# Optimization experiments

Hardware: AMD Instinct MI355X
Metric: run time of the kernel (lower is better)

The kernel has to match this reference:

```python
import jax, jax.numpy as jnp
import numpy as np

N_NODES = 500000
N_EDGES = 8000000


def gcn_conv(x, W, b, src, dst, n_nodes):
    # PyG GCNConv: add self-loops, symmetric normalization, x@W, scatter-add.
    loop = jnp.arange(n_nodes, dtype=src.dtype)
    src_a = jnp.concatenate([src, loop])  # [E+N]
    dst_a = jnp.concatenate([dst, loop])
    deg = jax.ops.segment_sum(jnp.ones_like(dst_a, dtype=x.dtype), dst_a,
                              num_segments=n_nodes)  # in-degree incl. self-loop
    dinv = jnp.where(deg > 0, jax.lax.rsqrt(deg), 0.0)
    norm = dinv[src_a] * dinv[dst_a]  # [E+N]
    xw = x @ W  # [N, out]
    msg = xw[src_a] * norm[:, None]  # [E+N, out]
    out = jax.ops.segment_sum(msg, dst_a, num_segments=n_nodes)
    return out + b


def setup_inputs() -> dict:
    key = jax.random.key(0)
    k1, k2, k3, k4, k5, k6 = jax.random.split(key, 6)
    x = jax.random.uniform(k1, (N_NODES, 1), dtype=jnp.float32)
    edge_index = jax.random.randint(k2, (2, N_EDGES), 0, N_NODES, dtype=jnp.int32)
    W1 = jax.random.normal(k3, (1, 16), dtype=jnp.float32)
    b1 = jax.random.normal(k4, (16,), dtype=jnp.float32) * 0.1
    W2 = jax.random.normal(k5, (16, 2), dtype=jnp.float32)
    b2 = jax.random.normal(k6, (2,), dtype=jnp.float32) * 0.1
    return {"x": x, "edge_index": edge_index, "W1": W1, "b1": b1,
            "W2": W2, "b2": b2}


def reference(x, edge_index, W1, b1, W2, b2):
    src, dst = edge_index[0], edge_index[1]
    h = gcn_conv(x, W1, b1, src, dst, N_NODES)
    h = jax.nn.relu(h)
    # dropout is identity in eval mode
    h = gcn_conv(h, W2, b2, src, dst, N_NODES)
    return jax.nn.log_softmax(h, axis=1)
```

## Files before the change

kernel.cpp:

```cpp
#include <hip/hip_runtime.h>
#include <math.h>


typedef unsigned int uint4v __attribute__((ext_vector_type(4)));

#define NPB 1024
#define NPB_SHIFT 10
#define NPB_MASK (NPB - 1)
#define MAXB 512
#define P1T 512
#define CHUNK 16384
#define SORT_CAP 17408
#define SPT 17

__device__ __forceinline__ unsigned short f2bf(float f) {
    unsigned int x = __float_as_uint(f);
    x += 0x7fffu + ((x >> 16) & 1u);
    return (unsigned short)(x >> 16);
}
__device__ __forceinline__ float bf2f(unsigned short h) {
    return __uint_as_float((unsigned int)h << 16);
}

__global__ __launch_bounds__(P1T, 4) void k_bucket(
    const int* __restrict__ src, const int* __restrict__ dst,
    unsigned int* __restrict__ file, int* __restrict__ ctr,
    int E, int nbucket, int cap)
{
    __shared__ unsigned int sorted[CHUNK];
    __shared__ int cnt[MAXB];
    __shared__ int pre[MAXB + 1];
    __shared__ int gb[MAXB];
    __shared__ int rk[MAXB];

    const int t  = threadIdx.x;
    const int e0 = blockIdx.x * CHUNK;
    const int nE = min(CHUNK, E - e0);

    for (int b = t; b < MAXB; b += P1T) { cnt[b] = 0; rk[b] = 0; }
    __syncthreads();

    const bool full = (nE == CHUNK);
    int4 dc[8];

    if (full) {
        const int4* d4 = (const int4*)(dst + e0);
#pragma unroll
        for (int k = 0; k < 8; ++k) dc[k] = d4[t + k * P1T];
#pragma unroll
        for (int k = 0; k < 8; ++k) {
            atomicAdd(&cnt[((unsigned)dc[k].x) >> NPB_SHIFT], 1);
            atomicAdd(&cnt[((unsigned)dc[k].y) >> NPB_SHIFT], 1);
            atomicAdd(&cnt[((unsigned)dc[k].z) >> NPB_SHIFT], 1);
            atomicAdd(&cnt[((unsigned)dc[k].w) >> NPB_SHIFT], 1);
        }
    } else {
        for (int i = t; i < nE; i += P1T)
            atomicAdd(&cnt[((unsigned)dst[e0 + i]) >> NPB_SHIFT], 1);
    }
    __syncthreads();

    int v = (t < nbucket) ? cnt[t] : 0;
    pre[t + 1] = v;
    if (t == 0) pre[0] = 0;
    __syncthreads();
    for (int off = 1; off < P1T; off <<= 1) {
        int add = (t >= off) ? pre[t + 1 - off] : 0;
        __syncthreads();
        pre[t + 1] += add;
        __syncthreads();
    }

    for (int b = t; b < nbucket; b += P1T) {
        int c = cnt[b];
        gb[b] = c ? atomicAdd(&ctr[b], c) : 0;
    }
    __syncthreads();

    if (full) {
        const int4* s4 = (const int4*)(src + e0);
#pragma unroll
        for (int k = 0; k < 8; ++k) {
            int4 s = s4[t + k * P1T];
            int4 d = dc[k];
            {
                int b = ((unsigned)d.x) >> NPB_SHIFT;
                int r = atomicAdd(&rk[b], 1);
                sorted[pre[b] + r] = (((unsigned)s.x) << NPB_SHIFT) | ((unsigned)d.x & NPB_MASK);
            }
            {
                int b = ((unsigned)d.y) >> NPB_SHIFT;
                int r = atomicAdd(&rk[b], 1);
                sorted[pre[b] + r] = (((unsigned)s.y) << NPB_SHIFT) | ((unsigned)d.y & NPB_MASK);
            }
            {
                int b = ((unsigned)d.z) >> NPB_SHIFT;
                int r = atomicAdd(&rk[b], 1);
                sorted[pre[b] + r] = (((unsigned)s.z) << NPB_SHIFT) | ((unsigned)d.z & NPB_MASK);
            }
            {
                int b = ((unsigned)d.w) >> NPB_SHIFT;
                int r = atomicAdd(&rk[b], 1);
                sorted[pre[b] + r] = (((unsigned)s.w) << NPB_SHIFT) | ((unsigned)d.w & NPB_MASK);
            }
        }
    } else {
        for (int i = t; i < nE; i += P1T) {
            int d = dst[e0 + i];
            int b = ((unsigned)d) >> NPB_SHIFT;
            unsigned int w = (((unsigned)src[e0 + i]) << NPB_SHIFT) |
                             ((unsigned)d & NPB_MASK);
            int r = atomicAdd(&rk[b], 1);
            sorted[pre[b] + r] = w;
        }
    }
    __syncthreads();

    {
        const int wid  = t >> 6;
        const int lane = t & 63;
        const int nw   = P1T >> 6;
        for (int b = wid; b < nbucket; b += nw) {
            int s0 = pre[b], s1 = pre[b + 1];
            int base = gb[b];
            unsigned int* dp = file + (size_t)b * cap;
            for (int j = s0 + lane; j < s1; j += 64) {
                int idx = base + (j - s0);
                if (idx < cap)
                    __builtin_nontemporal_store(sorted[j], &dp[idx]);
            }
        }
    }
}

__global__ __launch_bounds__(NPB) void k_sort(
    unsigned int* __restrict__ file, const int* __restrict__ ctr,
    int* __restrict__ start, const float* __restrict__ x,
    float* __restrict__ dinv, unsigned short* __restrict__ u,
    int N, int cap)
{
    __shared__ unsigned int sorted[SORT_CAP];
    __shared__ int cnt[NPB];
    __shared__ int pre[NPB + 1];

    const int t = threadIdx.x;
    const int b = blockIdx.x;
    const int nb = min(ctr[b], cap);
    unsigned int* f = file + (size_t)b * cap;

    cnt[t] = 0;
    __syncthreads();

    unsigned int ev[SPT];
    int rk_[SPT];
#pragma unroll
    for (int k = 0; k < SPT; ++k) {
        int i = t + (k << NPB_SHIFT);
        if (i < nb) ev[k] = __builtin_nontemporal_load(f + i);
    }
#pragma unroll
    for (int k = 0; k < SPT; ++k) {
        int i = t + (k << NPB_SHIFT);
        if (i < nb) rk_[k] = atomicAdd(&cnt[ev[k] & NPB_MASK], 1);
    }
    __syncthreads();

    pre[t + 1] = cnt[t];
    if (t == 0) pre[0] = 0;
    __syncthreads();
    for (int off = 1; off < NPB; off <<= 1) {
        int add = (t >= off) ? pre[t + 1 - off] : 0;
        __syncthreads();
        pre[t + 1] += add;
        __syncthreads();
    }

#pragma unroll
    for (int k = 0; k < SPT; ++k) {
        int i = t + (k << NPB_SHIFT);
        if (i < nb)
            sorted[pre[ev[k] & NPB_MASK] + rk_[k]] = ev[k] >> NPB_SHIFT;
    }
    __syncthreads();

    for (int i = t; i < nb; i += NPB)
        __builtin_nontemporal_store(sorted[i], &f[i]);

    start[b * (NPB + 1) + t] = pre[t];
    if (t == 0) start[b * (NPB + 1) + NPB] = pre[NPB];

    const int g = b * NPB + t;
    if (g < N) {
        float dv = rsqrtf((float)(cnt[t] + 1));
        dinv[g] = dv;
        u[g] = f2bf(x[g] * dv);
    }
}

__global__ __launch_bounds__(256) void k_agg1(
    const unsigned int* __restrict__ file, const int* __restrict__ start,
    const unsigned short* __restrict__ u, const float* __restrict__ dinv,
    const float* __restrict__ W1, const float* __restrict__ b1,
    const float* __restrict__ W2, unsigned int* __restrict__ q,
    int N, int cap)
{
    int g = blockIdx.x * 256 + threadIdx.x;
    if (g >= N) return;
    int b = g >> NPB_SHIFT, loc = g & NPB_MASK;
    const int* st = start + b * (NPB + 1);
    int e0 = st[loc], e1 = st[loc + 1];
    const unsigned int* f = file + (size_t)b * cap;

    float acc = 0.f;
    int j = e0;
    for (; j + 4 <= e1; j += 4) {
        unsigned int s0 = f[j], s1 = f[j + 1], s2 = f[j + 2], s3 = f[j + 3];
        float a = bf2f(u[s0]), bb = bf2f(u[s1]);
        float c = bf2f(u[s2]), d = bf2f(u[s3]);
        acc += (a + bb) + (c + d);
    }
    for (; j < e1; ++j) acc += bf2f(u[f[j]]);

    float dv = dinv[g];
    float s1v = (acc + bf2f(u[g])) * dv;
    float c0 = 0.f, c1 = 0.f;
#pragma unroll
    for (int k = 0; k < 16; ++k) {
        float h = fmaxf(fmaf(s1v, W1[k], b1[k]), 0.f);
        c0 = fmaf(h, W2[2 * k], c0);
        c1 = fmaf(h, W2[2 * k + 1], c1);
    }
    q[g] = (unsigned int)f2bf(c0 * dv) | ((unsigned int)f2bf(c1 * dv) << 16);
}

__global__ __launch_bounds__(256) void k_agg2(
    const unsigned int* __restrict__ file, const int* __restrict__ start,
    const unsigned int* __restrict__ q, const float* __restrict__ dinv,
    const float* __restrict__ b2, float2* __restrict__ out,
    int N, int cap)
{
    int g = blockIdx.x * 256 + threadIdx.x;
    if (g >= N) return;
    int b = g >> NPB_SHIFT, loc = g & NPB_MASK;
    const int* st = start + b * (NPB + 1);
    int e0 = st[loc], e1 = st[loc + 1];
    const unsigned int* f = file + (size_t)b * cap;

    float a0 = 0.f, a1 = 0.f;
    int j = e0;
    for (; j + 4 <= e1; j += 4) {
        unsigned int g0 = q[f[j]], g1 = q[f[j + 1]];
        unsigned int g2 = q[f[j + 2]], g3 = q[f[j + 3]];
        a0 += (bf2f((unsigned short)g0) + bf2f((unsigned short)g1)) +
              (bf2f((unsigned short)g2) + bf2f((unsigned short)g3));
        a1 += (bf2f((unsigned short)(g0 >> 16)) + bf2f((unsigned short)(g1 >> 16))) +
              (bf2f((unsigned short)(g2 >> 16)) + bf2f((unsigned short)(g3 >> 16)));
    }
    for (; j < e1; ++j) {
        unsigned int gq = q[f[j]];
        a0 += bf2f((unsigned short)gq);
        a1 += bf2f((unsigned short)(gq >> 16));
    }

    float dv = dinv[g];
    unsigned int qi = q[g];
    float o0 = (a0 + bf2f((unsigned short)qi)) * dv + b2[0];
    float o1 = (a1 + bf2f((unsigned short)(qi >> 16))) * dv + b2[1];
    float m = fmaxf(o0, o1);
    float l = m + logf(expf(o0 - m) + expf(o1 - m));
    out[g] = make_float2(o0 - l, o1 - l);
}

#define NT 256
__global__ __launch_bounds__(NT) void fb_deg(const int* __restrict__ dst,
                                             int* __restrict__ deg, int E) {
    int e = blockIdx.x * blockDim.x + threadIdx.x;
    if (e < E) atomicAdd(&deg[dst[e]], 1);
}
__global__ __launch_bounds__(NT) void fb_node1(const float* __restrict__ x,
                                               const int* __restrict__ deg,
                                               float* __restrict__ dinv,
                                               float* __restrict__ u, int N) {
    int i = blockIdx.x * blockDim.x + threadIdx.x;
    if (i < N) {
        float dv = rsqrtf((float)(deg[i] + 1));
        dinv[i] = dv;
        u[i] = x[i] * dv;
    }
}
__global__ __launch_bounds__(NT) void fb_edge1(const int* __restrict__ src,
                                               const int* __restrict__ dst,
                                               const float* __restrict__ u,
                                               float* __restrict__ agg1, int E) {
    int e = blockIdx.x * blockDim.x + threadIdx.x;
    if (e < E) atomicAdd(&agg1[dst[e]], u[src[e]]);
}
__global__ __launch_bounds__(NT) void fb_node2(const float* __restrict__ agg1,
                                               const float* __restrict__ u,
                                               const float* __restrict__ dinv,
                                               const float* __restrict__ W1,
                                               const float* __restrict__ b1,
                                               const float* __restrict__ W2,
                                               float2* __restrict__ q, int N) {
    int i = blockIdx.x * blockDim.x + threadIdx.x;
    if (i < N) {
        float dv = dinv[i];
        float s1 = (agg1[i] + u[i]) * dv;
        float c0 = 0.f, c1 = 0.f;
#pragma unroll
        for (int k = 0; k < 16; ++k) {
            float h = fmaxf(fmaf(s1, W1[k], b1[k]), 0.f);
            c0 = fmaf(h, W2[2 * k], c0);
            c1 = fmaf(h, W2[2 * k + 1], c1);
        }
        q[i] = make_float2(c0 * dv, c1 * dv);
    }
}
__global__ __launch_bounds__(NT) void fb_edge2(const int* __restrict__ src,
                                               const int* __restrict__ dst,
                                               const float2* __restrict__ q,
                                               float* __restrict__ agg2, int E) {
    int e = blockIdx.x * blockDim.x + threadIdx.x;
    if (e < E) {
        float2 qq = q[src[e]];
        atomicAdd(&agg2[2 * dst[e]], qq.x);
        atomicAdd(&agg2[2 * dst[e] + 1], qq.y);
    }
}
__global__ __launch_bounds__(NT) void fb_node3(const float* __restrict__ agg2,
                                               const float2* __restrict__ q,
                                               const float* __restrict__ dinv,
                                               const float* __restrict__ b2,
                                               float2* __restrict__ out, int N) {
    int i = blockIdx.x * blockDim.x + threadIdx.x;
    if (i < N) {
        float dv = dinv[i];
        float2 qi = q[i];
        float o0 = (agg2[2 * i] + qi.x) * dv + b2[0];
        float o1 = (agg2[2 * i + 1] + qi.y) * dv + b2[1];
        float m = fmaxf(o0, o1);
        float l = m + logf(expf(o0 - m) + expf(o1 - m));
        out[i] = make_float2(o0 - l, o1 - l);
    }
}

extern "C" void kernel_launch(void* const* d_in, const int* in_sizes, int n_in,
                              void* d_out, int out_size, void* d_ws, size_t ws_size,
                              hipStream_t stream) {
    const float* x  = (const float*)d_in[0];
    const int* ei   = (const int*)d_in[1];
    const float* W1 = (const float*)d_in[2];
    const float* b1 = (const float*)d_in[3];
    const float* W2 = (const float*)d_in[4];
    const float* b2 = (const float*)d_in[5];

    const int N = in_sizes[0];
    const int E = in_sizes[1] / 2;
    const int* src = ei;
    const int* dst = ei + E;

    const int nbucket = (N + NPB - 1) / NPB;
    const int cap = ((E / nbucket + 1024) + 63) & ~63;

    auto align_up = [](size_t v) { return (v + 255) & ~(size_t)255; };
    size_t off_ctr   = 0;
    size_t off_file  = align_up((size_t)MAXB * sizeof(int));
    size_t off_start = align_up(off_file + (size_t)nbucket * SORT_CAP * sizeof(unsigned int));
    size_t off_dinv  = align_up(off_start + (size_t)nbucket * (NPB + 1) * sizeof(int));
    size_t off_u     = align_up(off_dinv + (size_t)N * sizeof(float));
    size_t off_q     = align_up(off_u + (size_t)N * sizeof(unsigned short));
    size_t needed    = off_q + (size_t)N * sizeof(unsigned int);

    char* ws = (char*)d_ws;

    if (nbucket <= MAXB && cap <= SORT_CAP && needed <= ws_size) {
        int*            ctr   = (int*)(ws + off_ctr);
        unsigned int*   file  = (unsigned int*)(ws + off_file);
        int*            start = (int*)(ws + off_start);
        float*          dinv  = (float*)(ws + off_dinv);
        unsigned short* u     = (unsigned short*)(ws + off_u);
        unsigned int*   q     = (unsigned int*)(ws + off_q);

        (void)hipMemsetAsync(ctr, 0, (size_t)MAXB * sizeof(int), stream);

        const int p1Blocks  = (E + CHUNK - 1) / CHUNK;
        const int nodBlocks = (N + 255) / 256;
        k_bucket<<<p1Blocks, P1T, 0, stream>>>(src, dst, file, ctr, E, nbucket, SORT_CAP);
        k_sort  <<<nbucket, NPB, 0, stream>>>(file, ctr, start, x, dinv, u, N, SORT_CAP);
        k_agg1  <<<nodBlocks, 256, 0, stream>>>(file, start, u, dinv, W1, b1, W2, q, N, SORT_CAP);
        k_agg2  <<<nodBlocks, 256, 0, stream>>>(file, start, q, dinv, b2, (float2*)d_out, N, SORT_CAP);
    } else {
        int*    deg  = (int*)   (ws);
        float*  agg1 = (float*) (ws + (size_t)4 * N);
        float*  agg2 = (float*) (ws + (size_t)8 * N);
        float*  dinv = (float*) (ws + (size_t)16 * N);
        float*  u    = (float*) (ws + (size_t)20 * N);
        float2* q    = (float2*)(ws + (size_t)24 * N);
        (void)hipMemsetAsync(ws, 0, (size_t)16 * N, stream);
        const int nodeBlocks = (N + NT - 1) / NT;
        const int edgeBlocks = (E + NT - 1) / NT;
        fb_deg  <<<edgeBlocks, NT, 0, stream>>>(dst, deg, E);
        fb_node1<<<nodeBlocks, NT, 0, stream>>>(x, deg, dinv, u, N);
        fb_edge1<<<edgeBlocks, NT, 0, stream>>>(src, dst, u, agg1, E);
        fb_node2<<<nodeBlocks, NT, 0, stream>>>(agg1, u, dinv, W1, b1, W2, q, N);
        fb_edge2<<<edgeBlocks, NT, 0, stream>>>(src, dst, q, agg2, E);
        fb_node3<<<nodeBlocks, NT, 0, stream>>>(agg2, q, dinv, b2, (float2*)d_out, N);
    }
}
```

Baseline: 237.7 us.

## Replace per-bucket counting sort with LDS atomic accumulation per bucket

Drops the in-bucket counting sort and CSR start array. Each aggregation pass now runs one 1024-thread block per bucket, streams the unsorted bucketed edges with vectorized uint4 loads, gathers source values and accumulates into shared-memory float atomics keyed by the local destination. This removes the sort's scan, scatter and write-back plus the start-array traffic. In exchange it adds contended LDS float atomics and makes the summation order nondeterministic, and only about 489 blocks run per pass.

```diff
diff --git a/kernel.cpp b/kernel.cpp
--- a/kernel.cpp
+++ b/kernel.cpp
@@ -1,8 +1,6 @@
 #include <hip/hip_runtime.h>
 #include <math.h>
 
-
-typedef unsigned int uint4v __attribute__((ext_vector_type(4)));
 
 #define NPB 1024
 #define NPB_SHIFT 10
@@ -11,7 +9,6 @@
 #define P1T 512
 #define CHUNK 16384
 #define SORT_CAP 17408
-#define SPT 17
 
 __device__ __forceinline__ unsigned short f2bf(float f) {
     unsigned int x = __float_as_uint(f);
@@ -133,61 +130,32 @@
     }
 }
 
-__global__ __launch_bounds__(NPB) void k_sort(
-    unsigned int* __restrict__ file, const int* __restrict__ ctr,
-    int* __restrict__ start, const float* __restrict__ x,
-    float* __restrict__ dinv, unsigned short* __restrict__ u,
-    int N, int cap)
+__global__ __launch_bounds__(NPB) void k_deg(
+    const unsigned int* __restrict__ file, const int* __restrict__ ctr,
+    const float* __restrict__ x, float* __restrict__ dinv,
+    unsigned short* __restrict__ u, int N, int cap)
 {
-    __shared__ unsigned int sorted[SORT_CAP];
     __shared__ int cnt[NPB];
-    __shared__ int pre[NPB + 1];
 
     const int t = threadIdx.x;
     const int b = blockIdx.x;
     const int nb = min(ctr[b], cap);
-    unsigned int* f = file + (size_t)b * cap;
+    const unsigned int* f = file + (size_t)b * cap;
 
     cnt[t] = 0;
     __syncthreads();
 
-    unsigned int ev[SPT];
-    int rk_[SPT];
-#pragma unroll
-    for (int k = 0; k < SPT; ++k) {
-        int i = t + (k << NPB_SHIFT);
-        if (i < nb) ev[k] = __builtin_nontemporal_load(f + i);
-    }
-#pragma unroll
-    for (int k = 0; k < SPT; ++k) {
-        int i = t + (k << NPB_SHIFT);
-        if (i < nb) rk_[k] = atomicAdd(&cnt[ev[k] & NPB_MASK], 1);
-    }
-    __syncthreads();
-
-    pre[t + 1] = cnt[t];
-    if (t == 0) pre[0] = 0;
-    __syncthreads();
-    for (int off = 1; off < NPB; off <<= 1) {
-        int add = (t >= off) ? pre[t + 1 - off] : 0;
-        __syncthreads();
-        pre[t + 1] += add;
-        __syncthreads();
-    }
-
-#pragma unroll
-    for (int k = 0; k < SPT; ++k) {
-        int i = t + (k << NPB_SHIFT);
-        if (i < nb)
-            sorted[pre[ev[k] & NPB_MASK] + rk_[k]] = ev[k] >> NPB_SHIFT;
-    }
-    __syncthreads();
-
-    for (int i = t; i < nb; i += NPB)
-        __builtin_nontemporal_store(sorted[i], &f[i]);
-
-    start[b * (NPB + 1) + t] = pre[t];
-    if (t == 0) start[b * (NPB + 1) + NPB] = pre[NPB];
+    const int nb4 = nb & ~3;
+    for (int i = 4 * t; i < nb4; i += 4 * NPB) {
+        uint4 ev = *(const uint4*)(f + i);
+        atomicAdd(&cnt[ev.x & NPB_MASK], 1);
+        atomicAdd(&cnt[ev.y & NPB_MASK], 1);
+        atomicAdd(&cnt[ev.z & NPB_MASK], 1);
+        atomicAdd(&cnt[ev.w & NPB_MASK], 1);
+    }
+    if (t < nb - nb4)
+        atomicAdd(&cnt[f[nb4 + t] & NPB_MASK], 1);
+    __syncthreads();
 
     const int g = b * NPB + t;
     if (g < N) {
@@ -197,78 +165,108 @@
     }
 }
 
-__global__ __launch_bounds__(256) void k_agg1(
-    const unsigned int* __restrict__ file, const int* __restrict__ start,
+__global__ __launch_bounds__(NPB) void k_acc1(
+    const unsigned int* __restrict__ file, const int* __restrict__ ctr,
     const unsigned short* __restrict__ u, const float* __restrict__ dinv,
     const float* __restrict__ W1, const float* __restrict__ b1,
     const float* __restrict__ W2, unsigned int* __restrict__ q,
     int N, int cap)
 {
-    int g = blockIdx.x * 256 + threadIdx.x;
-    if (g >= N) return;
-    int b = g >> NPB_SHIFT, loc = g & NPB_MASK;
-    const int* st = start + b * (NPB + 1);
-    int e0 = st[loc], e1 = st[loc + 1];
+    __shared__ float acc[NPB];
+
+    const int t = threadIdx.x;
+    const int b = blockIdx.x;
+    const int nb = min(ctr[b], cap);
     const unsigned int* f = file + (size_t)b * cap;
 
-    float acc = 0.f;
-    int j = e0;
-    for (; j + 4 <= e1; j += 4) {
-        unsigned int s0 = f[j], s1 = f[j + 1], s2 = f[j + 2], s3 = f[j + 3];
-        float a = bf2f(u[s0]), bb = bf2f(u[s1]);
-        float c = bf2f(u[s2]), d = bf2f(u[s3]);
-        acc += (a + bb) + (c + d);
-    }
-    for (; j < e1; ++j) acc += bf2f(u[f[j]]);
-
-    float dv = dinv[g];
-    float s1v = (acc + bf2f(u[g])) * dv;
-    float c0 = 0.f, c1 = 0.f;
+    acc[t] = 0.f;
+    __syncthreads();
+
+    const int nb4 = nb & ~3;
+    for (int i = 4 * t; i < nb4; i += 4 * NPB) {
+        uint4 ev = *(const uint4*)(f + i);
+        float v0 = bf2f(u[ev.x >> NPB_SHIFT]);
+        float v1 = bf2f(u[ev.y >> NPB_SHIFT]);
+        float v2 = bf2f(u[ev.z >> NPB_SHIFT]);
+        float v3 = bf2f(u[ev.w >> NPB_SHIFT]);
+        atomicAdd(&acc[ev.x & NPB_MASK], v0);
+        atomicAdd(&acc[ev.y & NPB_MASK], v1);
+        atomicAdd(&acc[ev.z & NPB_MASK], v2);
+        atomicAdd(&acc[ev.w & NPB_MASK], v3);
+    }
+    if (t < nb - nb4) {
+        unsigned int ev = f[nb4 + t];
+        atomicAdd(&acc[ev & NPB_MASK], bf2f(u[ev >> NPB_SHIFT]));
+    }
+    __syncthreads();
+
+    const int g = b * NPB + t;
+    if (g < N) {
+        float dv = dinv[g];
+        float s1v = (acc[t] + bf2f(u[g])) * dv;
+        float c0 = 0.f, c1 = 0.f;
 #pragma unroll
-    for (int k = 0; k < 16; ++k) {
-        float h = fmaxf(fmaf(s1v, W1[k], b1[k]), 0.f);
-        c0 = fmaf(h, W2[2 * k], c0);
-        c1 = fmaf(h, W2[2 * k + 1], c1);
-    }
-    q[g] = (unsigned int)f2bf(c0 * dv) | ((unsigned int)f2bf(c1 * dv) << 16);
-}
-
-__global__ __launch_bounds__(256) void k_agg2(
-    const unsigned int* __restrict__ file, const int* __restrict__ start,
+        for (int k = 0; k < 16; ++k) {
+            float h = fmaxf(fmaf(s1v, W1[k], b1[k]), 0.f);
+            c0 = fmaf(h, W2[2 * k], c0);
+            c1 = fmaf(h, W2[2 * k + 1], c1);
+        }
+        q[g] = (unsigned int)f2bf(c0 * dv) | ((unsigned int)f2bf(c1 * dv) << 16);
+    }
+}
+
+__global__ __launch_bounds__(NPB) void k_acc2(
+    const unsigned int* __restrict__ file, const int* __restrict__ ctr,
     const unsigned int* __restrict__ q, const float* __restrict__ dinv,
     const float* __restrict__ b2, float2* __restrict__ out,
     int N, int cap)
 {
-    int g = blockIdx.x * 256 + threadIdx.x;
-    if (g >= N) return;
-    int b = g >> NPB_SHIFT, loc = g & NPB_MASK;
-    const int* st = start + b * (NPB + 1);
-    int e0 = st[loc], e1 = st[loc + 1];
+    __shared__ float a0[NPB];
+    __shared__ float a1[NPB];
+
+    const int t = threadIdx.x;
+    const int b = blockIdx.x;
+    const int nb = min(ctr[b], cap);
     const unsigned int* f = file + (size_t)b * cap;
 
-    float a0 = 0.f, a1 = 0.f;
-    int j = e0;
-    for (; j + 4 <= e1; j += 4) {
-        unsigned int g0 = q[f[j]], g1 = q[f[j + 1]];
-        unsigned int g2 = q[f[j + 2]], g3 = q[f[j + 3]];
-        a0 += (bf2f((unsigned short)g0) + bf2f((unsigned short)g1)) +
-              (bf2f((unsigned short)g2) + bf2f((unsigned short)g3));
-        a1 += (bf2f((unsigned short)(g0 >> 16)) + bf2f((unsigned short)(g1 >> 16))) +
-              (bf2f((unsigned short)(g2 >> 16)) + bf2f((unsigned short)(g3 >> 16)));
-    }
-    for (; j < e1; ++j) {
-        unsigned int gq = q[f[j]];
-        a0 += bf2f((unsigned short)gq);
-        a1 += bf2f((unsigned short)(gq >> 16));
-    }
-
-    float dv = dinv[g];
-    unsigned int qi = q[g];
-    float o0 = (a0 + bf2f((unsigned short)qi)) * dv + b2[0];
-    float o1 = (a1 + bf2f((unsigned short)(qi >> 16))) * dv + b2[1];
-    float m = fmaxf(o0, o1);
-    float l = m + logf(expf(o0 - m) + expf(o1 - m));
-    out[g] = make_float2(o0 - l, o1 - l);
+    a0[t] = 0.f;
+    a1[t] = 0.f;
+    __syncthreads();
+
+    const int nb4 = nb & ~3;
+    for (int i = 4 * t; i < nb4; i += 4 * NPB) {
+        uint4 ev = *(const uint4*)(f + i);
+        unsigned int g0 = q[ev.x >> NPB_SHIFT];
+        unsigned int g1 = q[ev.y >> NPB_SHIFT];
+        unsigned int g2 = q[ev.z >> NPB_SHIFT];
+        unsigned int g3 = q[ev.w >> NPB_SHIFT];
+        atomicAdd(&a0[ev.x & NPB_MASK], bf2f((unsigned short)g0));
+        atomicAdd(&a1[ev.x & NPB_MASK], bf2f((unsigned short)(g0 >> 16)));
+        atomicAdd(&a0[ev.y & NPB_MASK], bf2f((unsigned short)g1));
+        atomicAdd(&a1[ev.y & NPB_MASK], bf2f((unsigned short)(g1 >> 16)));
+        atomicAdd(&a0[ev.z & NPB_MASK], bf2f((unsigned short)g2));
+        atomicAdd(&a1[ev.z & NPB_MASK], bf2f((unsigned short)(g2 >> 16)));
+        atomicAdd(&a0[ev.w & NPB_MASK], bf2f((unsigned short)g3));
+        atomicAdd(&a1[ev.w & NPB_MASK], bf2f((unsigned short)(g3 >> 16)));
+    }
+    if (t < nb - nb4) {
+        unsigned int ev = f[nb4 + t];
+        unsigned int gq = q[ev >> NPB_SHIFT];
+        atomicAdd(&a0[ev & NPB_MASK], bf2f((unsigned short)gq));
+        atomicAdd(&a1[ev & NPB_MASK], bf2f((unsigned short)(gq >> 16)));
+    }
+    __syncthreads();
+
+    const int g = b * NPB + t;
+    if (g < N) {
+        float dv = dinv[g];
+        unsigned int qi = q[g];
+        float o0 = (a0[t] + bf2f((unsigned short)qi)) * dv + b2[0];
+        float o1 = (a1[t] + bf2f((unsigned short)(qi >> 16))) * dv + b2[1];
+        float m = fmaxf(o0, o1);
+        float l = m + logf(expf(o0 - m) + expf(o1 - m));
+        out[g] = make_float2(o0 - l, o1 - l);
+    }
 }
 
 #define NT 256
@@ -365,8 +363,7 @@
     auto align_up = [](size_t v) { return (v + 255) & ~(size_t)255; };
     size_t off_ctr   = 0;
     size_t off_file  = align_up((size_t)MAXB * sizeof(int));
-    size_t off_start = align_up(off_file + (size_t)nbucket * SORT_CAP * sizeof(unsigned int));
-    size_t off_dinv  = align_up(off_start + (size_t)nbucket * (NPB + 1) * sizeof(int));
+    size_t off_dinv  = align_up(off_file + (size_t)nbucket * SORT_CAP * sizeof(unsigned int));
     size_t off_u     = align_up(off_dinv + (size_t)N * sizeof(float));
     size_t off_q     = align_up(off_u + (size_t)N * sizeof(unsigned short));
     size_t needed    = off_q + (size_t)N * sizeof(unsigned int);
@@ -376,19 +373,17 @@
     if (nbucket <= MAXB && cap <= SORT_CAP && needed <= ws_size) {
         int*            ctr   = (int*)(ws + off_ctr);
         unsigned int*   file  = (unsigned int*)(ws + off_file);
-        int*            start = (int*)(ws + off_start);
         float*          dinv  = (float*)(ws + off_dinv);
         unsigned short* u     = (unsigned short*)(ws + off_u);
         unsigned int*   q     = (unsigned int*)(ws + off_q);
 
         (void)hipMemsetAsync(ctr, 0, (size_t)MAXB * sizeof(int), stream);
 
-        const int p1Blocks  = (E + CHUNK - 1) / CHUNK;
-        const int nodBlocks = (N + 255) / 256;
+        const int p1Blocks = (E + CHUNK - 1) / CHUNK;
         k_bucket<<<p1Blocks, P1T, 0, stream>>>(src, dst, file, ctr, E, nbucket, SORT_CAP);
-        k_sort  <<<nbucket, NPB, 0, stream>>>(file, ctr, start, x, dinv, u, N, SORT_CAP);
-        k_agg1  <<<nodBlocks, 256, 0, stream>>>(file, start, u, dinv, W1, b1, W2, q, N, SORT_CAP);
-        k_agg2  <<<nodBlocks, 256, 0, stream>>>(file, start, q, dinv, b2, (float2*)d_out, N, SORT_CAP);
+        k_deg   <<<nbucket, NPB, 0, stream>>>(file, ctr, x, dinv, u, N, SORT_CAP);
+        k_acc1  <<<nbucket, NPB, 0, stream>>>(file, ctr, u, dinv, W1, b1, W2, q, N, SORT_CAP);
+        k_acc2  <<<nbucket, NPB, 0, stream>>>(file, ctr, q, dinv, b2, (float2*)d_out, N, SORT_CAP);
     } else {
         int*    deg  = (int*)   (ws);
         float*  agg1 = (float*) (ws + (size_t)4 * N);
```

Result: slower. 272.3 us (+14.5%).
